# Kernel tuning notes

Hardware: AMD Instinct MI355X
Metric: run time of the kernel (lower is better)

The kernel has to match this reference:

```python
import jax, jax.numpy as jnp
import numpy as np

# mamba-2.8b layer dims
B_, L = 2, 2048
D_MODEL = 2560
D_IN = 2 * D_MODEL          # 5120, d_inner
N = 16                      # d_state
DT_RANK = D_MODEL // 16     # 160


def setup_inputs() -> dict:
    key = jax.random.key(0)
    ks = jax.random.split(key, 6)
    x = jax.random.normal(ks[0], (B_, L, D_IN), dtype=jnp.float32)
    # A_log initialized so A = -exp(A_log) in [-16, -1], as in Mamba's S4D-real init
    A_log = jnp.log(jax.random.uniform(ks[1], (D_IN, N), minval=1.0, maxval=16.0, dtype=jnp.float32))
    D = jax.random.normal(ks[2], (D_IN,), dtype=jnp.float32) * 0.1 + 1.0
    x_proj_w = jax.random.normal(ks[3], (DT_RANK + 2 * N, D_IN), dtype=jnp.float32) * (D_IN ** -0.5)
    dt_proj_w = jax.random.normal(ks[4], (D_IN, DT_RANK), dtype=jnp.float32) * (DT_RANK ** -0.5)
    dt_proj_b = jax.random.normal(ks[5], (D_IN,), dtype=jnp.float32) * 0.1
    return {"x": x, "A_log": A_log, "D": D, "x_proj_w": x_proj_w,
            "dt_proj_w": dt_proj_w, "dt_proj_b": dt_proj_b}


def _ssm(x, A_log, D, x_proj_w, dt_proj_w, dt_proj_b):
    # x: (b, l, d_inner)
    A = -jnp.exp(A_log)                                        # (d, n)
    x_dbl = jnp.einsum('bld,ed->ble', x, x_proj_w)             # (b, l, dt_rank+2n)
    dt_raw = x_dbl[..., :DT_RANK]                              # (b, l, dt_rank)
    Bm = x_dbl[..., DT_RANK:DT_RANK + N]                       # (b, l, n)
    Cm = x_dbl[..., DT_RANK + N:]                              # (b, l, n)
    delta = jax.nn.softplus(jnp.einsum('blr,dr->bld', dt_raw, dt_proj_w) + dt_proj_b)  # (b, l, d)

    def step(h, inp):
        xt, dt, Bt, Ct = inp                                   # (b,d) (b,d) (b,n) (b,n)
        dA = jnp.exp(dt[..., None] * A)                        # (b, d, n)
        h = dA * h + (dt * xt)[..., None] * Bt[:, None, :]     # (b, d, n)
        y = jnp.einsum('bdn,bn->bd', h, Ct)                    # (b, d)
        return h, y

    xs = (jnp.swapaxes(x, 0, 1), jnp.swapaxes(delta, 0, 1),
          jnp.swapaxes(Bm, 0, 1), jnp.swapaxes(Cm, 0, 1))
    h0 = jnp.zeros((x.shape[0], D_IN, N), dtype=x.dtype)
    _, ys = jax.lax.scan(step, h0, xs)                         # ys: (l, b, d)
    return jnp.swapaxes(ys, 0, 1) + x * D                      # (b, l, d)


def reference(x, A_log, D, x_proj_w, dt_proj_w, dt_proj_b):
    return _ssm(x, A_log, D, x_proj_w, dt_proj_w, dt_proj_b)
```

## Files before the change

### kernel.cpp

```cpp
#include <hip/hip_runtime.h>
#include <hip/hip_bf16.h>

#define DIN   5120
#define LSEQ  2048
#define BATCH 2
#define MROWS 4096
#define EOUT  192
#define RDT   160
#define NST   16
#define NC    64
#define LC    32
#define LOG2E 1.44269504088896f
#define LN2   0.69314718055995f

typedef __attribute__((ext_vector_type(8))) short bf16x8;
typedef __attribute__((ext_vector_type(4))) float f32x4;

__device__ __forceinline__ void stdelta(float* p, size_t i, float v) { p[i] = v; }
__device__ __forceinline__ void stdelta(__hip_bfloat16* p, size_t i, float v) { p[i] = __float2bfloat16(v); }
__device__ __forceinline__ float lddelta(const float* p, size_t i) { return p[i]; }
__device__ __forceinline__ float lddelta(const __hip_bfloat16* p, size_t i) { return __bfloat162float(p[i]); }

__device__ __forceinline__ float softplus_fast(float v) {
    float t = __builtin_amdgcn_exp2f(-fabsf(v) * LOG2E);
    return fmaxf(v, 0.f) + __builtin_amdgcn_logf(1.f + t) * LN2;
}
__device__ __forceinline__ unsigned short bf16rne(float f) {
    unsigned int u = __float_as_uint(f);
    unsigned int r = (u + 0x7FFFu + ((u >> 16) & 1u)) >> 16;
    return (unsigned short)r;
}
__device__ __forceinline__ void cvt8(float4 a, float4 b, bf16x8& h, bf16x8& l) {
    float v[8] = {a.x, a.y, a.z, a.w, b.x, b.y, b.z, b.w};
    #pragma unroll
    for (int e = 0; e < 8; e++) {
        __hip_bfloat16 hb = __float2bfloat16(v[e]);
        float hf = __bfloat162float(hb);
        __hip_bfloat16 lb = __float2bfloat16(v[e] - hf);
        h[e] = *reinterpret_cast<const short*>(&hb);
        l[e] = *reinterpret_cast<const short*>(&lb);
    }
}

__global__ void k0_cvtw(const float* __restrict__ w, ushort* __restrict__ bw) {
    int i = blockIdx.x * 256 + threadIdx.x;
    float4 v = reinterpret_cast<const float4*>(w)[i];
    ushort4 o = make_ushort4(bf16rne(v.x), bf16rne(v.y), bf16rne(v.z), bf16rne(v.w));
    reinterpret_cast<ushort4*>(bw)[i] = o;
}

template <int KPS>
__global__ __launch_bounds__(256) void k1_mfma(const float* __restrict__ x,
                                               const ushort* __restrict__ bWp,
                                               float* __restrict__ part) {
    const int tid = threadIdx.x;
    const int m_base = blockIdx.x * 64;
    const int k_base = blockIdx.y * KPS;
    const int lane = tid & 63, w = tid >> 6;
    const int lr = lane & 15, lg = lane >> 4;
    const int wm = m_base + w * 16;

    f32x4 acc[12];
    #pragma unroll
    for (int j = 0; j < 12; j++) acc[j] = (f32x4)(0.f);

    const float* xr = x + (size_t)(wm + lr) * DIN + k_base + lg * 8;
    const ushort* br = bWp + (size_t)lr * DIN + k_base + lg * 8;

    for (int kk = 0; kk < KPS / 32; kk++) {
        const int ko = kk * 32;
        bf16x8 bb[12];
        #pragma unroll
        for (int j = 0; j < 12; j++)
            bb[j] = *reinterpret_cast<const bf16x8*>(br + (size_t)j * 16 * DIN + ko);
        float4 v0 = *reinterpret_cast<const float4*>(xr + ko);
        float4 v1 = *reinterpret_cast<const float4*>(xr + ko + 4);
        bf16x8 ah, al;
        cvt8(v0, v1, ah, al);
        #pragma unroll
        for (int j = 0; j < 12; j++) {
            acc[j] = __builtin_amdgcn_mfma_f32_16x16x32_bf16(ah, bb[j], acc[j], 0, 0, 0);
            acc[j] = __builtin_amdgcn_mfma_f32_16x16x32_bf16(al, bb[j], acc[j], 0, 0, 0);
        }
    }
    float* p = part + (size_t)blockIdx.y * MROWS * EOUT;
    #pragma unroll
    for (int j = 0; j < 12; j++) {
        const int e = j * 16 + lr;
        const int m0 = wm + lg * 4;
        #pragma unroll
        for (int r = 0; r < 4; r++)
            p[(size_t)(m0 + r) * EOUT + e] = acc[j][r];
    }
}

template <int KS>
__global__ void k1_reduce(const float* __restrict__ part, float* __restrict__ xdbl,
                          ushort* __restrict__ aHi, ushort* __restrict__ aLo) {
    int i = blockIdx.x * 256 + threadIdx.x;
    const float4* p = reinterpret_cast<const float4*>(part);
    float4 s = p[i];
    #pragma unroll
    for (int k = 1; k < KS; k++) {
        float4 v = p[(size_t)k * (MROWS * EOUT / 4) + i];
        s.x += v.x; s.y += v.y; s.z += v.z; s.w += v.w;
    }
    reinterpret_cast<float4*>(xdbl)[i] = s;
    int row = i / 48, e4 = i % 48;
    if (e4 < 40) {
        unsigned int hx = __float_as_uint(s.x) & 0xFFFF0000u;
        unsigned int hy = __float_as_uint(s.y) & 0xFFFF0000u;
        unsigned int hz = __float_as_uint(s.z) & 0xFFFF0000u;
        unsigned int hw = __float_as_uint(s.w) & 0xFFFF0000u;
        ushort4 hv = make_ushort4((unsigned short)(hx >> 16), (unsigned short)(hy >> 16),
                                  (unsigned short)(hz >> 16), (unsigned short)(hw >> 16));
        ushort4 lv = make_ushort4(bf16rne(s.x - __uint_as_float(hx)),
                                  bf16rne(s.y - __uint_as_float(hy)),
                                  bf16rne(s.z - __uint_as_float(hz)),
                                  bf16rne(s.w - __uint_as_float(hw)));
        *reinterpret_cast<ushort4*>(&aHi[(size_t)row * RDT + e4 * 4]) = hv;
        *reinterpret_cast<ushort4*>(&aLo[(size_t)row * RDT + e4 * 4]) = lv;
    }
}

template <typename DT>
__global__ __launch_bounds__(256, 3) void k2_mfma(const ushort* __restrict__ aHi,
                                                  const ushort* __restrict__ aLo,
                                                  const ushort* __restrict__ bW,
                                                  const float* __restrict__ bias,
                                                  DT* __restrict__ delta) {
    const int tid = threadIdx.x;
    const int m_base = blockIdx.x * 64, d_base = blockIdx.y * 256;
    const int lane = tid & 63, w = tid >> 6;
    const int wr = w >> 1, wc = w & 1;
    const int lr = lane & 15, lg = lane >> 4;

    f32x4 acc[2][8];
    #pragma unroll
    for (int i = 0; i < 2; i++)
        #pragma unroll
        for (int j = 0; j < 8; j++) acc[i][j] = (f32x4)(0.f);

    const size_t arow = (size_t)(m_base + wr * 32 + lr) * RDT;
    const size_t brow = (size_t)(d_base + wc * 128 + lr) * RDT;

    #pragma unroll
    for (int kk = 0; kk < 5; kk++) {
        const int ko = kk * 32 + lg * 8;
        bf16x8 ah0 = *reinterpret_cast<const bf16x8*>(aHi + arow + ko);
        bf16x8 ah1 = *reinterpret_cast<const bf16x8*>(aHi + arow + 16 * RDT + ko);
        bf16x8 al0 = *reinterpret_cast<const bf16x8*>(aLo + arow + ko);
        bf16x8 al1 = *reinterpret_cast<const bf16x8*>(aLo + arow + 16 * RDT + ko);
        #pragma unroll
        for (int j = 0; j < 8; j++) {
            bf16x8 bb = *reinterpret_cast<const bf16x8*>(bW + brow + (size_t)j * 16 * RDT + ko);
            acc[0][j] = __builtin_amdgcn_mfma_f32_16x16x32_bf16(ah0, bb, acc[0][j], 0, 0, 0);
            acc[1][j] = __builtin_amdgcn_mfma_f32_16x16x32_bf16(ah1, bb, acc[1][j], 0, 0, 0);
            acc[0][j] = __builtin_amdgcn_mfma_f32_16x16x32_bf16(al0, bb, acc[0][j], 0, 0, 0);
            acc[1][j] = __builtin_amdgcn_mfma_f32_16x16x32_bf16(al1, bb, acc[1][j], 0, 0, 0);
        }
    }

    #pragma unroll
    for (int j = 0; j < 8; j++) {
        const int gd = d_base + wc * 128 + j * 16 + lr;
        const float bv = bias[gd];
        #pragma unroll
        for (int i = 0; i < 2; i++) {
            const int gm0 = m_base + wr * 32 + i * 16 + lg * 4;
            #pragma unroll
            for (int r = 0; r < 4; r++) {
                float v = acc[i][j][r] + bv;
                stdelta(delta, (size_t)(gm0 + r) * DIN + gd, softplus_fast(v));
            }
        }
    }
}

template <typename DT>
__global__ __launch_bounds__(256) void k3a_local(const float* __restrict__ x,
                                                 const DT* __restrict__ delta,
                                                 const float* __restrict__ xdbl,
                                                 const float* __restrict__ A_log,
                                                 float* __restrict__ Sbuf,
                                                 float* __restrict__ hboth) {
    const int tid = threadIdx.x;
    const int d = blockIdx.x * 256 + tid;
    const int c = blockIdx.y, b = blockIdx.z;

    float4 aq[4];
    #pragma unroll
    for (int q = 0; q < 4; q++) aq[q] = *reinterpret_cast<const float4*>(&A_log[d * NST + q * 4]);
    const float* av = reinterpret_cast<const float*>(aq);
    float A2[NST];
    #pragma unroll
    for (int n = 0; n < NST; n++) A2[n] = -expf(av[n]) * LOG2E;

    float h[NST];
    #pragma unroll
    for (int n = 0; n < NST; n++) h[n] = 0.f;
    float S = 0.f;

    const size_t gbase = (size_t)b * LSEQ * DIN + (size_t)c * LC * DIN + d;
    const float* Bbase = xdbl + ((size_t)b * LSEQ + (size_t)c * LC) * EOUT + RDT;

    float dv = lddelta(delta, gbase);
    float xv = x[gbase];
    float4 bq[4];
    {
        const float4* Bp = reinterpret_cast<const float4*>(Bbase);
        bq[0] = Bp[0]; bq[1] = Bp[1]; bq[2] = Bp[2]; bq[3] = Bp[3];
    }
    for (int tt = 0; tt < LC; tt++) {
        const int ttn = (tt + 1 < LC) ? tt + 1 : tt;
        float dv_n = lddelta(delta, gbase + (size_t)ttn * DIN);
        float xv_n = x[gbase + (size_t)ttn * DIN];
        float4 bqn[4];
        {
            const float4* Bp = reinterpret_cast<const float4*>(Bbase + (size_t)ttn * EOUT);
            bqn[0] = Bp[0]; bqn[1] = Bp[1]; bqn[2] = Bp[2]; bqn[3] = Bp[3];
        }
        const float* Bv = reinterpret_cast<const float*>(bq);
        S += dv;
        const float dvx = dv * xv;
        #pragma unroll
        for (int n = 0; n < NST; n++)
            h[n] = fmaf(__builtin_amdgcn_exp2f(dv * A2[n]), h[n], dvx * Bv[n]);
        dv = dv_n; xv = xv_n;
        bq[0] = bqn[0]; bq[1] = bqn[1]; bq[2] = bqn[2]; bq[3] = bqn[3];
    }
    Sbuf[((size_t)b * NC + c) * DIN + d] = S;
    float* hp = hboth + (((size_t)b * NC + c) * DIN + d) * NST;
    #pragma unroll
    for (int q = 0; q < 4; q++)
        reinterpret_cast<float4*>(hp)[q] = make_float4(h[q*4], h[q*4+1], h[q*4+2], h[q*4+3]);
}

__global__ __launch_bounds__(256) void k3b_combine(const float* __restrict__ Sbuf,
                                                   float* __restrict__ hboth,
                                                   const float* __restrict__ A_log) {
    const int i = blockIdx.x * 256 + threadIdx.x;
    const int b = i / (DIN * 4);
    const int r = i % (DIN * 4);
    const int d = r >> 2, q = r & 3;
    float4 av = *reinterpret_cast<const float4*>(&A_log[d * NST + q * 4]);
    float A2x = -expf(av.x) * LOG2E, A2y = -expf(av.y) * LOG2E;
    float A2z = -expf(av.z) * LOG2E, A2w = -expf(av.w) * LOG2E;
    float4 hi = make_float4(0.f, 0.f, 0.f, 0.f);
    float4* hb4 = reinterpret_cast<float4*>(hboth);
    for (int c = 0; c < NC; c++) {
        const size_t idx4 = (((size_t)b * NC + c) * DIN + d) * 4 + q;
        float4 he = hb4[idx4];
        float S = Sbuf[((size_t)b * NC + c) * DIN + d];
        hb4[idx4] = hi;
        hi.x = fmaf(__builtin_amdgcn_exp2f(S * A2x), hi.x, he.x);
        hi.y = fmaf(__builtin_amdgcn_exp2f(S * A2y), hi.y, he.y);
        hi.z = fmaf(__builtin_amdgcn_exp2f(S * A2z), hi.z, he.z);
        hi.w = fmaf(__builtin_amdgcn_exp2f(S * A2w), hi.w, he.w);
    }
}

template <typename DT>
__global__ __launch_bounds__(256) void k3c_scan(const float* __restrict__ x,
                                                const DT* __restrict__ delta,
                                                const float* __restrict__ xdbl,
                                                const float* __restrict__ A_log,
                                                const float* __restrict__ Dw,
                                                const float* __restrict__ hboth,
                                                float* __restrict__ out) {
    const int tid = threadIdx.x;
    const int d = blockIdx.x * 256 + tid;
    const int c = blockIdx.y, b = blockIdx.z;

    float4 aq[4];
    #pragma unroll
    for (int q = 0; q < 4; q++) aq[q] = *reinterpret_cast<const float4*>(&A_log[d * NST + q * 4]);
    const float* av = reinterpret_cast<const float*>(aq);
    float A2[NST];
    #pragma unroll
    for (int n = 0; n < NST; n++) A2[n] = -expf(av[n]) * LOG2E;

    float h[NST];
    {
        const float* hp = hboth + (((size_t)b * NC + c) * DIN + d) * NST;
        float4 hq[4];
        #pragma unroll
        for (int q = 0; q < 4; q++) hq[q] = reinterpret_cast<const float4*>(hp)[q];
        const float* hv = reinterpret_cast<const float*>(hq);
        #pragma unroll
        for (int n = 0; n < NST; n++) h[n] = hv[n];
    }
    const float Dv = Dw[d];

    const size_t gbase = (size_t)b * LSEQ * DIN + (size_t)c * LC * DIN + d;
    const float* Bbase = xdbl + ((size_t)b * LSEQ + (size_t)c * LC) * EOUT + RDT;

    float dv = lddelta(delta, gbase);
    float xv = x[gbase];
    float4 bq[4], cq[4];
    {
        const float4* Bp = reinterpret_cast<const float4*>(Bbase);
        bq[0] = Bp[0]; bq[1] = Bp[1]; bq[2] = Bp[2]; bq[3] = Bp[3];
        cq[0] = Bp[4]; cq[1] = Bp[5]; cq[2] = Bp[6]; cq[3] = Bp[7];
    }
    for (int tt = 0; tt < LC; tt++) {
        const int ttn = (tt + 1 < LC) ? tt + 1 : tt;
        float dv_n = lddelta(delta, gbase + (size_t)ttn * DIN);
        float xv_n = x[gbase + (size_t)ttn * DIN];
        float4 bqn[4], cqn[4];
        {
            const float4* Bp = reinterpret_cast<const float4*>(Bbase + (size_t)ttn * EOUT);
            bqn[0] = Bp[0]; bqn[1] = Bp[1]; bqn[2] = Bp[2]; bqn[3] = Bp[3];
            cqn[0] = Bp[4]; cqn[1] = Bp[5]; cqn[2] = Bp[6]; cqn[3] = Bp[7];
        }
        const float* Bv = reinterpret_cast<const float*>(bq);
        const float* Cv = reinterpret_cast<const float*>(cq);
        const float dvx = dv * xv;
        float y0 = 0.f, y1 = 0.f, y2 = 0.f, y3 = 0.f;
        #pragma unroll
        for (int n = 0; n < NST; n += 4) {
            h[n+0] = fmaf(__builtin_amdgcn_exp2f(dv * A2[n+0]), h[n+0], dvx * Bv[n+0]);
            y0 = fmaf(h[n+0], Cv[n+0], y0);
            h[n+1] = fmaf(__builtin_amdgcn_exp2f(dv * A2[n+1]), h[n+1], dvx * Bv[n+1]);
            y1 = fmaf(h[n+1], Cv[n+1], y1);
            h[n+2] = fmaf(__builtin_amdgcn_exp2f(dv * A2[n+2]), h[n+2], dvx * Bv[n+2]);
            y2 = fmaf(h[n+2], Cv[n+2], y2);
            h[n+3] = fmaf(__builtin_amdgcn_exp2f(dv * A2[n+3]), h[n+3], dvx * Bv[n+3]);
            y3 = fmaf(h[n+3], Cv[n+3], y3);
        }
        out[gbase + (size_t)tt * DIN] = ((y0 + y1) + (y2 + y3)) + xv * Dv;
        dv = dv_n; xv = xv_n;
        bq[0] = bqn[0]; bq[1] = bqn[1]; bq[2] = bqn[2]; bq[3] = bqn[3];
        cq[0] = cqn[0]; cq[1] = cqn[1]; cq[2] = cqn[2]; cq[3] = cqn[3];
    }
}

extern "C" void kernel_launch(void* const* d_in, const int* in_sizes, int n_in,
                              void* d_out, int out_size, void* d_ws, size_t ws_size,
                              hipStream_t stream) {
    const float* x     = (const float*)d_in[0];
    const float* A_log = (const float*)d_in[1];
    const float* Dw    = (const float*)d_in[2];
    const float* xpw   = (const float*)d_in[3];
    const float* dtw   = (const float*)d_in[4];
    const float* dtb   = (const float*)d_in[5];
    float* out = (float*)d_out;

    char* ws = (char*)d_ws;
    size_t off = 0;
    float* xdbl  = (float*)(ws + off); off += (size_t)MROWS * EOUT * 4;
    float* hboth = (float*)(ws + off); off += (size_t)BATCH * NC * DIN * NST * 4;
    float* Sbuf  = (float*)(ws + off); off += (size_t)BATCH * NC * DIN * 4;
    ushort* aHi  = (ushort*)(ws + off); off += (size_t)MROWS * RDT * 2;
    ushort* aLo  = (ushort*)(ws + off); off += (size_t)MROWS * RDT * 2;
    ushort* bW   = (ushort*)(ws + off); off += (size_t)DIN * RDT * 2;
    ushort* bWp  = (ushort*)(ws + off); off += (size_t)EOUT * DIN * 2;
    const size_t delta_off = off;
    const bool f32ok = ws_size >= delta_off + (size_t)MROWS * DIN * 4;

    k0_cvtw<<<dim3(EOUT * DIN / 4 / 256), 256, 0, stream>>>(xpw, bWp);
    k0_cvtw<<<dim3(DIN * RDT / 4 / 256), 256, 0, stream>>>(dtw, bW);

    if (f32ok) {
        float* part = (float*)(ws + delta_off);
        float* delta = (float*)(ws + delta_off);
        k1_mfma<DIN / 16><<<dim3(MROWS / 64, 16), 256, 0, stream>>>(x, bWp, part);
        k1_reduce<16><<<dim3(MROWS * EOUT / 4 / 256), 256, 0, stream>>>(part, xdbl, aHi, aLo);
        k2_mfma<float><<<dim3(MROWS / 64, DIN / 256), 256, 0, stream>>>(aHi, aLo, bW, dtb, delta);
        k3a_local<float><<<dim3(DIN / 256, NC, BATCH), 256, 0, stream>>>(x, delta, xdbl, A_log, Sbuf, hboth);
        k3b_combine<<<dim3(BATCH * DIN * 4 / 256), 256, 0, stream>>>(Sbuf, hboth, A_log);
        k3c_scan<float><<<dim3(DIN / 256, NC, BATCH), 256, 0, stream>>>(x, delta, xdbl, A_log, Dw, hboth, out);
    } else {
        float* part = hboth;
        __hip_bfloat16* delta = (__hip_bfloat16*)(ws + delta_off);
        k1_mfma<DIN / 8><<<dim3(MROWS / 64, 8), 256, 0, stream>>>(x, bWp, part);
        k1_reduce<8><<<dim3(MROWS * EOUT / 4 / 256), 256, 0, stream>>>(part, xdbl, aHi, aLo);
        k2_mfma<__hip_bfloat16><<<dim3(MROWS / 64, DIN / 256), 256, 0, stream>>>(aHi, aLo, bW, dtb, delta);
        k3a_local<__hip_bfloat16><<<dim3(DIN / 256, NC, BATCH), 256, 0, stream>>>(x, delta, xdbl, A_log, Sbuf, hboth);
        k3b_combine<<<dim3(BATCH * DIN * 4 / 256), 256, 0, stream>>>(Sbuf, hboth, A_log);
        k3c_scan<__hip_bfloat16><<<dim3(DIN / 256, NC, BATCH), 256, 0, stream>>>(x, delta, xdbl, A_log, Dw, hboth, out);
    }
}
```

Before: 256.9 us.

## Pre-pack MFMA B fragments and stage x tiles through swizzled LDS

Weight conversion kernels now write bf16 weights in MFMA fragment order, so each lane's B loads in k1 and k2 are contiguous 16-byte chunks across a wave instead of strided row reads. k1 double-buffers 64x64 fp32 x tiles in XOR-swizzled shared memory with coalesced row loads, replacing direct per-lane strided global reads. k2 hoists its eight B fragment loads ahead of the MFMA loop. The aim is better coalescing and latency hiding in the projection GEMMs, at the cost of 32KB of LDS per k1 block and extra barriers.

Result: faster. 227.5 us (-11.4%).

```diff
diff --git a/kernel.cpp b/kernel.cpp
--- a/kernel.cpp
+++ b/kernel.cpp
@@ -12,6 +12,8 @@
 #define LC    32
 #define LOG2E 1.44269504088896f
 #define LN2   0.69314718055995f
+#define KB1   (DIN / 32)
+#define KB2   (RDT / 32)
 
 typedef __attribute__((ext_vector_type(8))) short bf16x8;
 typedef __attribute__((ext_vector_type(4))) float f32x4;
@@ -42,46 +44,79 @@
     }
 }
 
-__global__ void k0_cvtw(const float* __restrict__ w, ushort* __restrict__ bw) {
-    int i = blockIdx.x * 256 + threadIdx.x;
-    float4 v = reinterpret_cast<const float4*>(w)[i];
-    ushort4 o = make_ushort4(bf16rne(v.x), bf16rne(v.y), bf16rne(v.z), bf16rne(v.w));
-    reinterpret_cast<ushort4*>(bw)[i] = o;
-}
-
+template <int K>
+__global__ void k0_packB(const float* __restrict__ w, ushort* __restrict__ bP) {
+    const int KBl = K / 32;
+    int p = blockIdx.x * 256 + threadIdx.x;
+    int lr = p & 15, lg = (p >> 4) & 3;
+    int kkg = (p >> 6) % KBl, j = p / (64 * KBl);
+    const float* src = w + (size_t)(j * 16 + lr) * K + kkg * 32 + lg * 8;
+    float4 a = *reinterpret_cast<const float4*>(src);
+    float4 b = *reinterpret_cast<const float4*>(src + 4);
+    ushort o[8] = {bf16rne(a.x), bf16rne(a.y), bf16rne(a.z), bf16rne(a.w),
+                   bf16rne(b.x), bf16rne(b.y), bf16rne(b.z), bf16rne(b.w)};
+    ushort* dst = bP + (size_t)p * 8;
+    *reinterpret_cast<ushort4*>(dst)     = make_ushort4(o[0], o[1], o[2], o[3]);
+    *reinterpret_cast<ushort4*>(dst + 4) = make_ushort4(o[4], o[5], o[6], o[7]);
+}
+
+#define K1_BK 64
 template <int KPS>
 __global__ __launch_bounds__(256) void k1_mfma(const float* __restrict__ x,
-                                               const ushort* __restrict__ bWp,
+                                               const ushort* __restrict__ bP,
                                                float* __restrict__ part) {
+    __shared__ float xs[2][64 * 64];
     const int tid = threadIdx.x;
     const int m_base = blockIdx.x * 64;
     const int k_base = blockIdx.y * KPS;
     const int lane = tid & 63, w = tid >> 6;
     const int lr = lane & 15, lg = lane >> 4;
-    const int wm = m_base + w * 16;
+    const int wm = w * 16;
 
     f32x4 acc[12];
     #pragma unroll
     for (int j = 0; j < 12; j++) acc[j] = (f32x4)(0.f);
 
-    const float* xr = x + (size_t)(wm + lr) * DIN + k_base + lg * 8;
-    const ushort* br = bWp + (size_t)lr * DIN + k_base + lg * 8;
-
-    for (int kk = 0; kk < KPS / 32; kk++) {
-        const int ko = kk * 32;
-        bf16x8 bb[12];
-        #pragma unroll
-        for (int j = 0; j < 12; j++)
-            bb[j] = *reinterpret_cast<const bf16x8*>(br + (size_t)j * 16 * DIN + ko);
-        float4 v0 = *reinterpret_cast<const float4*>(xr + ko);
-        float4 v1 = *reinterpret_cast<const float4*>(xr + ko + 4);
-        bf16x8 ah, al;
-        cvt8(v0, v1, ah, al);
-        #pragma unroll
-        for (int j = 0; j < 12; j++) {
-            acc[j] = __builtin_amdgcn_mfma_f32_16x16x32_bf16(ah, bb[j], acc[j], 0, 0, 0);
-            acc[j] = __builtin_amdgcn_mfma_f32_16x16x32_bf16(al, bb[j], acc[j], 0, 0, 0);
-        }
+    const int srow4 = tid >> 4, scol = tid & 15;
+
+    auto stage = [&](int buf, int kc) {
+        #pragma unroll
+        for (int p = 0; p < 4; p++) {
+            int row = p * 16 + srow4;
+            float4 v = *reinterpret_cast<const float4*>(
+                &x[(size_t)(m_base + row) * DIN + k_base + kc + scol * 4]);
+            *reinterpret_cast<float4*>(&xs[buf][row * 64 + ((scol ^ (row & 7)) * 4)]) = v;
+        }
+    };
+
+    stage(0, 0);
+    const ushort* bpl = bP + ((size_t)lg * 16 + lr) * 8;
+    __syncthreads();
+
+    int buf = 0;
+    for (int kc = 0; kc < KPS; kc += K1_BK) {
+        if (kc + K1_BK < KPS) stage(buf ^ 1, kc + K1_BK);
+        #pragma unroll
+        for (int kk = 0; kk < K1_BK / 32; kk++) {
+            const int kglob = (k_base + kc) / 32 + kk;
+            bf16x8 bb[12];
+            #pragma unroll
+            for (int j = 0; j < 12; j++)
+                bb[j] = *reinterpret_cast<const bf16x8*>(bpl + ((size_t)j * KB1 + kglob) * 512);
+            const int row = wm + lr;
+            const int ca = kk * 8 + lg * 2;
+            float4 f0 = *reinterpret_cast<const float4*>(&xs[buf][row * 64 + ((ca ^ (row & 7)) * 4)]);
+            float4 f1 = *reinterpret_cast<const float4*>(&xs[buf][row * 64 + (((ca + 1) ^ (row & 7)) * 4)]);
+            bf16x8 ah, al;
+            cvt8(f0, f1, ah, al);
+            #pragma unroll
+            for (int j = 0; j < 12; j++) {
+                acc[j] = __builtin_amdgcn_mfma_f32_16x16x32_bf16(ah, bb[j], acc[j], 0, 0, 0);
+                acc[j] = __builtin_amdgcn_mfma_f32_16x16x32_bf16(al, bb[j], acc[j], 0, 0, 0);
+            }
+        }
+        __syncthreads();
+        buf ^= 1;
     }
     float* p = part + (size_t)blockIdx.y * MROWS * EOUT;
     #pragma unroll
@@ -90,7 +125,7 @@
         const int m0 = wm + lg * 4;
         #pragma unroll
         for (int r = 0; r < 4; r++)
-            p[(size_t)(m0 + r) * EOUT + e] = acc[j][r];
+            p[(size_t)(m_base + m0 + r) * EOUT + e] = acc[j][r];
     }
 }
 
@@ -126,7 +161,7 @@
 template <typename DT>
 __global__ __launch_bounds__(256, 3) void k2_mfma(const ushort* __restrict__ aHi,
                                                   const ushort* __restrict__ aLo,
-                                                  const ushort* __restrict__ bW,
+                                                  const ushort* __restrict__ bP2,
                                                   const float* __restrict__ bias,
                                                   DT* __restrict__ delta) {
     const int tid = threadIdx.x;
@@ -142,7 +177,8 @@
         for (int j = 0; j < 8; j++) acc[i][j] = (f32x4)(0.f);
 
     const size_t arow = (size_t)(m_base + wr * 32 + lr) * RDT;
-    const size_t brow = (size_t)(d_base + wc * 128 + lr) * RDT;
+    const int jt_base = d_base / 16 + wc * 8;
+    const ushort* bpl = bP2 + ((size_t)lg * 16 + lr) * 8;
 
     #pragma unroll
     for (int kk = 0; kk < 5; kk++) {
@@ -151,13 +187,16 @@
         bf16x8 ah1 = *reinterpret_cast<const bf16x8*>(aHi + arow + 16 * RDT + ko);
         bf16x8 al0 = *reinterpret_cast<const bf16x8*>(aLo + arow + ko);
         bf16x8 al1 = *reinterpret_cast<const bf16x8*>(aLo + arow + 16 * RDT + ko);
+        bf16x8 bb[8];
+        #pragma unroll
+        for (int j = 0; j < 8; j++)
+            bb[j] = *reinterpret_cast<const bf16x8*>(bpl + ((size_t)(jt_base + j) * KB2 + kk) * 512);
         #pragma unroll
         for (int j = 0; j < 8; j++) {
-            bf16x8 bb = *reinterpret_cast<const bf16x8*>(bW + brow + (size_t)j * 16 * RDT + ko);
-            acc[0][j] = __builtin_amdgcn_mfma_f32_16x16x32_bf16(ah0, bb, acc[0][j], 0, 0, 0);
-            acc[1][j] = __builtin_amdgcn_mfma_f32_16x16x32_bf16(ah1, bb, acc[1][j], 0, 0, 0);
-            acc[0][j] = __builtin_amdgcn_mfma_f32_16x16x32_bf16(al0, bb, acc[0][j], 0, 0, 0);
-            acc[1][j] = __builtin_amdgcn_mfma_f32_16x16x32_bf16(al1, bb, acc[1][j], 0, 0, 0);
+            acc[0][j] = __builtin_amdgcn_mfma_f32_16x16x32_bf16(ah0, bb[j], acc[0][j], 0, 0, 0);
+            acc[1][j] = __builtin_amdgcn_mfma_f32_16x16x32_bf16(ah1, bb[j], acc[1][j], 0, 0, 0);
+            acc[0][j] = __builtin_amdgcn_mfma_f32_16x16x32_bf16(al0, bb[j], acc[0][j], 0, 0, 0);
+            acc[1][j] = __builtin_amdgcn_mfma_f32_16x16x32_bf16(al1, bb[j], acc[1][j], 0, 0, 0);
         }
     }
 
@@ -353,29 +392,29 @@
     float* Sbuf  = (float*)(ws + off); off += (size_t)BATCH * NC * DIN * 4;
     ushort* aHi  = (ushort*)(ws + off); off += (size_t)MROWS * RDT * 2;
     ushort* aLo  = (ushort*)(ws + off); off += (size_t)MROWS * RDT * 2;
-    ushort* bW   = (ushort*)(ws + off); off += (size_t)DIN * RDT * 2;
-    ushort* bWp  = (ushort*)(ws + off); off += (size_t)EOUT * DIN * 2;
+    ushort* bP2  = (ushort*)(ws + off); off += (size_t)DIN * RDT * 2;
+    ushort* bP1  = (ushort*)(ws + off); off += (size_t)EOUT * DIN * 2;
     const size_t delta_off = off;
     const bool f32ok = ws_size >= delta_off + (size_t)MROWS * DIN * 4;
 
-    k0_cvtw<<<dim3(EOUT * DIN / 4 / 256), 256, 0, stream>>>(xpw, bWp);
-    k0_cvtw<<<dim3(DIN * RDT / 4 / 256), 256, 0, stream>>>(dtw, bW);
+    k0_packB<DIN><<<dim3(EOUT * DIN / 8 / 256), 256, 0, stream>>>(xpw, bP1);
+    k0_packB<RDT><<<dim3(DIN * RDT / 8 / 256), 256, 0, stream>>>(dtw, bP2);
 
     if (f32ok) {
         float* part = (float*)(ws + delta_off);
         float* delta = (float*)(ws + delta_off);
-        k1_mfma<DIN / 16><<<dim3(MROWS / 64, 16), 256, 0, stream>>>(x, bWp, part);
+        k1_mfma<DIN / 16><<<dim3(MROWS / 64, 16), 256, 0, stream>>>(x, bP1, part);
         k1_reduce<16><<<dim3(MROWS * EOUT / 4 / 256), 256, 0, stream>>>(part, xdbl, aHi, aLo);
-        k2_mfma<float><<<dim3(MROWS / 64, DIN / 256), 256, 0, stream>>>(aHi, aLo, bW, dtb, delta);
+        k2_mfma<float><<<dim3(MROWS / 64, DIN / 256), 256, 0, stream>>>(aHi, aLo, bP2, dtb, delta);
         k3a_local<float><<<dim3(DIN / 256, NC, BATCH), 256, 0, stream>>>(x, delta, xdbl, A_log, Sbuf, hboth);
         k3b_combine<<<dim3(BATCH * DIN * 4 / 256), 256, 0, stream>>>(Sbuf, hboth, A_log);
         k3c_scan<float><<<dim3(DIN / 256, NC, BATCH), 256, 0, stream>>>(x, delta, xdbl, A_log, Dw, hboth, out);
     } else {
         float* part = hboth;
         __hip_bfloat16* delta = (__hip_bfloat16*)(ws + delta_off);
-        k1_mfma<DIN / 8><<<dim3(MROWS / 64, 8), 256, 0, stream>>>(x, bWp, part);
+        k1_mfma<DIN / 8><<<dim3(MROWS / 64, 8), 256, 0, stream>>>(x, bP1, part);
         k1_reduce<8><<<dim3(MROWS * EOUT / 4 / 256), 256, 0, stream>>>(part, xdbl, aHi, aLo);
-        k2_mfma<__hip_bfloat16><<<dim3(MROWS / 64, DIN / 256), 256, 0, stream>>>(aHi, aLo, bW, dtb, delta);
+        k2_mfma<__hip_bfloat16><<<dim3(MROWS / 64, DIN / 256), 256, 0, stream>>>(aHi, aLo, bP2, dtb, delta);
         k3a_local<__hip_bfloat16><<<dim3(DIN / 256, NC, BATCH), 256, 0, stream>>>(x, delta, xdbl, A_log, Sbuf, hboth);
         k3b_combine<<<dim3(BATCH * DIN * 4 / 256), 256, 0, stream>>>(Sbuf, hboth, A_log);
         k3c_scan<__hip_bfloat16><<<dim3(DIN / 256, NC, BATCH), 256, 0, stream>>>(x, delta, xdbl, A_log, Dw, hboth, out);
```
